# Kernel tuning notes

Measured on AMD Instinct MI355X. Metric: run time of the kernel, lower is better.

## Reference

```python
import jax, jax.numpy as jnp
import numpy as np

B, V, E, W = 1024, 50257, 128, 4  # batch, vocab, embed, CBOW window

def setup_inputs() -> dict:
    key = jax.random.key(0)
    k1, k2, k3, k4 = jax.random.split(key, 4)
    # near-one-hot averaged bag-of-words: 2*W context indices per row, each weighted 1/(2*W)
    ctx_idx = jax.random.randint(k1, (B, 2 * W), 0, V)
    xs = jnp.zeros((B, V), dtype=jnp.float32).at[jnp.arange(B)[:, None], ctx_idx].add(1.0 / (2 * W))
    metric = jax.random.normal(k2, (E, E), dtype=jnp.float32)  # unused by forward, kept for signature fidelity
    EMBEDM = jax.random.normal(k3, (V, E), dtype=jnp.float32)
    embed2vocab = jax.random.normal(k4, (E, V), dtype=jnp.float32)
    return {"xs": xs, "metric": metric, "EMBEDM": EMBEDM, "embed2vocab": embed2vocab}

def reference(xs, metric, EMBEDM, embed2vocab):
    # [B,V] @ [V,E] -> [B,E]  (gather+average in disguise: xs is sparse n-hot)
    xsembeds = xs @ EMBEDM
    # [B,E] @ [E,V] -> [B,V], then row-wise log_softmax
    xsouts = xsembeds @ embed2vocab
    return jax.nn.log_softmax(xsouts, axis=1)
```

## Files before the change

kernel.cpp:

```cpp
#include <hip/hip_runtime.h>
#include <hip/hip_bf16.h>

#define B_ROWS 1024
#define V_DIM 50257
#define E_DIM 128
#define V_PAD 50304
#define NCT 786

typedef __attribute__((ext_vector_type(8))) short short8;
typedef __attribute__((ext_vector_type(4))) float float4v;

__global__ void k0_transpose(const float* __restrict__ e2v,
                             __hip_bfloat16* __restrict__ e2vT) {
    __shared__ float t[32][33];
    const int v0 = blockIdx.x * 32;
    const int k0 = blockIdx.y * 32;
    const int c = threadIdx.x & 31;
    const int r = threadIdx.x >> 5;
#pragma unroll
    for (int i = 0; i < 4; ++i) {
        const int k = k0 + r + i * 8;
        const int v = v0 + c;
        t[r + i * 8][c] = (v < V_DIM) ? e2v[(size_t)k * V_DIM + v] : 0.0f;
    }
    __syncthreads();
#pragma unroll
    for (int i = 0; i < 4; ++i) {
        const int rv = r + i * 8;
        e2vT[(size_t)(v0 + rv) * E_DIM + k0 + c] = __float2bfloat16(t[c][rv]);
    }
}

__global__ void k1_embed(const float* __restrict__ xs,
                         const float* __restrict__ EM,
                         __hip_bfloat16* __restrict__ xse) {
    const int b = blockIdx.x;
    const int tid = threadIdx.x;
    __shared__ int nzv[64];
    __shared__ float nzval[64];
    __shared__ int nzcount;
    if (tid == 0) nzcount = 0;
    __syncthreads();

    const size_t base = (size_t)b * V_DIM;
    auto note = [&](int v, float val) {
        if (val != 0.0f) {
            int s = atomicAdd(&nzcount, 1);
            if (s < 64) { nzv[s] = v; nzval[s] = val; }
        }
    };

    const int h = (int)((4 - (base & 3)) & 3);
    if (tid < h) note(tid, xs[base + tid]);
    const int n4 = (V_DIM - h) >> 2;
    const float4* xv = reinterpret_cast<const float4*>(xs + base + h);
#pragma unroll 4
    for (int j = tid; j < n4; j += 256) {
        float4 x = xv[j];
        if (x.x != 0.0f || x.y != 0.0f || x.z != 0.0f || x.w != 0.0f) {
            const int v = h + 4 * j;
            note(v + 0, x.x);
            note(v + 1, x.y);
            note(v + 2, x.z);
            note(v + 3, x.w);
        }
    }
    for (int i = h + n4 * 4 + tid; i < V_DIM; i += 256) note(i, xs[base + i]);
    __syncthreads();

    int cnt = nzcount;
    if (cnt > 64) cnt = 64;
    if (tid < E_DIM) {
        float a = 0.0f;
        for (int s = 0; s < cnt; ++s)
            a += nzval[s] * EM[(size_t)nzv[s] * E_DIM + tid];
        xse[(size_t)b * E_DIM + tid] = __float2bfloat16(a);
    }
}

template <bool PASS2>
__global__ __launch_bounds__(256) void gemm_tile(
        const __hip_bfloat16* __restrict__ xse,
        const __hip_bfloat16* __restrict__ e2vT,
        float* __restrict__ psum,
        const float* __restrict__ stats,
        float* __restrict__ out) {
    __shared__ __align__(16) unsigned short Bs[64][136];
    const int tid = threadIdx.x;
    const int v0 = blockIdx.x * 64;
    const int m0 = blockIdx.y * 128;

    const unsigned short* gA = reinterpret_cast<const unsigned short*>(xse);
    const unsigned short* gB = reinterpret_cast<const unsigned short*>(e2vT);

    int4 g[4];
#pragma unroll
    for (int i = 0; i < 4; ++i) {
        const int p = tid + i * 256;
        const int row = p >> 4;
        const int kc = (p & 15) << 3;
        g[i] = *reinterpret_cast<const int4*>(gB + (size_t)(v0 + row) * E_DIM + kc);
    }

    const int w = tid >> 6;
    const int lane = tid & 63;
    const int q = lane >> 4;
    const int l16 = lane & 15;
    const int wm = w * 32;

    short8 af[2][4];
#pragma unroll
    for (int mi = 0; mi < 2; ++mi)
#pragma unroll
        for (int kt = 0; kt < 4; ++kt)
            af[mi][kt] = *reinterpret_cast<const short8*>(
                gA + (size_t)(m0 + wm + mi * 16 + l16) * E_DIM + kt * 32 + q * 8);

#pragma unroll
    for (int i = 0; i < 4; ++i) {
        const int p = tid + i * 256;
        const int row = p >> 4;
        const int kc = (p & 15) << 3;
        *reinterpret_cast<int4*>(&Bs[row][kc]) = g[i];
    }
    __syncthreads();

    float4v acc[2][4];
#pragma unroll
    for (int mi = 0; mi < 2; ++mi)
#pragma unroll
        for (int ni = 0; ni < 4; ++ni)
            acc[mi][ni] = (float4v){0.0f, 0.0f, 0.0f, 0.0f};

#pragma unroll
    for (int kt = 0; kt < 4; ++kt) {
        const int ko = kt * 32 + q * 8;
#pragma unroll
        for (int ni = 0; ni < 4; ++ni) {
            short8 bf = *reinterpret_cast<const short8*>(&Bs[ni * 16 + l16][ko]);
            acc[0][ni] = __builtin_amdgcn_mfma_f32_16x16x32_bf16(af[0][kt], bf, acc[0][ni], 0, 0, 0);
            acc[1][ni] = __builtin_amdgcn_mfma_f32_16x16x32_bf16(af[1][kt], bf, acc[1][ni], 0, 0, 0);
        }
    }

    if constexpr (!PASS2) {
        const bool full = (v0 + 64 <= V_DIM);
#pragma unroll
        for (int mi = 0; mi < 2; ++mi) {
#pragma unroll
            for (int r = 0; r < 4; ++r) {
                float s;
                if (full) {
                    s = __expf(acc[mi][0][r]) + __expf(acc[mi][1][r]) +
                        __expf(acc[mi][2][r]) + __expf(acc[mi][3][r]);
                } else {
                    s = 0.0f;
#pragma unroll
                    for (int ni = 0; ni < 4; ++ni)
                        if (v0 + ni * 16 + l16 < V_DIM) s += __expf(acc[mi][ni][r]);
                }
                s += __shfl_xor(s, 1);
                s += __shfl_xor(s, 2);
                s += __shfl_xor(s, 4);
                s += __shfl_xor(s, 8);
                if (l16 == 0) {
                    const int row = m0 + wm + mi * 16 + q * 4 + r;
                    psum[(size_t)row * NCT + blockIdx.x] = s;
                }
            }
        }
    } else {
#pragma unroll
        for (int mi = 0; mi < 2; ++mi) {
            const int rbase = m0 + wm + mi * 16 + q * 4;
            float l[4];
#pragma unroll
            for (int r = 0; r < 4; ++r) l[r] = stats[rbase + r];
#pragma unroll
            for (int ni = 0; ni < 4; ++ni) {
                const int col = v0 + ni * 16 + l16;
                if (col < V_DIM) {
#pragma unroll
                    for (int r = 0; r < 4; ++r)
                        out[(size_t)(rbase + r) * V_DIM + col] = acc[mi][ni][r] - l[r];
                }
            }
        }
    }
}

__global__ void kc_combine(const float* __restrict__ psum,
                           float* __restrict__ stats) {
    const int b = blockIdx.x;
    const int lane = threadIdx.x;
    float s = 0.0f;
    for (int j = lane; j < NCT; j += 64) s += psum[(size_t)b * NCT + j];
#pragma unroll
    for (int d = 1; d < 64; d <<= 1) s += __shfl_xor(s, d);
    if (lane == 0) stats[b] = __logf(s);
}

extern "C" void kernel_launch(void* const* d_in, const int* in_sizes, int n_in,
                              void* d_out, int out_size, void* d_ws, size_t ws_size,
                              hipStream_t stream) {
    const float* xs  = (const float*)d_in[0];
    const float* EM  = (const float*)d_in[2];
    const float* e2v = (const float*)d_in[3];
    float* out = (float*)d_out;

    char* ws = (char*)d_ws;
    __hip_bfloat16* e2vT = (__hip_bfloat16*)ws;
    size_t off = (size_t)V_PAD * E_DIM * 2;
    __hip_bfloat16* xse = (__hip_bfloat16*)(ws + off);
    off += (size_t)B_ROWS * E_DIM * 2;
    float* psum = (float*)(ws + off);
    off += (size_t)B_ROWS * NCT * 4;
    float* stats = (float*)(ws + off);

    k0_transpose<<<dim3(V_PAD / 32, E_DIM / 32), dim3(256), 0, stream>>>(e2v, e2vT);
    k1_embed<<<dim3(B_ROWS), dim3(256), 0, stream>>>(xs, EM, xse);
    gemm_tile<false><<<dim3(NCT, B_ROWS / 128), dim3(256), 0, stream>>>(
        xse, e2vT, psum, nullptr, nullptr);
    kc_combine<<<dim3(B_ROWS), dim3(64), 0, stream>>>(psum, stats);
    gemm_tile<true><<<dim3(NCT, B_ROWS / 128), dim3(256), 0, stream>>>(
        xse, e2vT, nullptr, stats, out);
}
```

Baseline: 472.3 us.

## Fuse all stages into one persistent cooperative kernel with grid syncs

Replaces the five separate launches (transpose, embed, sum pass, combine, output pass) with a single cooperative persistent kernel that steps through the stages with grid-wide syncs. Each block handles a contiguous range of jobs ordered so consecutive jobs reuse the same vocab tile already loaded in shared memory, which avoids reloading the B tile for all 8 row panels. The aim is to remove launch gaps and tail effects between kernels. The cost is grid-sync overhead, a grid capped at 1024 blocks, and higher shared-memory use per block. The old multi-kernel path remains as a fallback if the cooperative launch fails.

New measurement: 673.9 us. 42.7% more time.

```diff
diff --git a/kernel.cpp b/kernel.cpp
--- a/kernel.cpp
+++ b/kernel.cpp
@@ -1,14 +1,262 @@
 #include <hip/hip_runtime.h>
 #include <hip/hip_bf16.h>
+#include <hip/hip_cooperative_groups.h>
+
+namespace cg = cooperative_groups;
 
 #define B_ROWS 1024
 #define V_DIM 50257
 #define E_DIM 128
 #define V_PAD 50304
 #define NCT 786
+#define NPANEL 8
+#define NJOBS (NCT * NPANEL)
+#define NTX 1572
+#define NTJOBS (NTX * 4)
+#define MAXGRID 1024
 
 typedef __attribute__((ext_vector_type(8))) short short8;
 typedef __attribute__((ext_vector_type(4))) float float4v;
+
+__global__ __launch_bounds__(256, 4) void fused(
+        const float* __restrict__ xs,
+        const float* __restrict__ EM,
+        const float* __restrict__ e2v,
+        __hip_bfloat16* __restrict__ e2vT,
+        __hip_bfloat16* __restrict__ xse,
+        float* __restrict__ psum,
+        float* __restrict__ stats,
+        float* __restrict__ out) {
+    __shared__ __align__(16) unsigned short Bs[64][136];
+    __shared__ float t[32][33];
+    __shared__ int nzv[64];
+    __shared__ float nzval[64];
+    __shared__ int nzcount;
+
+    const int bid = blockIdx.x;
+    const int nblk = gridDim.x;
+    const int tid = threadIdx.x;
+    const int w = tid >> 6;
+    const int lane = tid & 63;
+    const int q = lane >> 4;
+    const int l16 = lane & 15;
+    const int wm = w * 32;
+    cg::grid_group gg = cg::this_grid();
+
+    for (int job = bid; job < NTJOBS; job += nblk) {
+        const int y = job / NTX;
+        const int x = job - y * NTX;
+        const int v0 = x * 32, k0 = y * 32;
+        const int c = tid & 31, r = tid >> 5;
+#pragma unroll
+        for (int i = 0; i < 4; ++i) {
+            const int k = k0 + r + i * 8;
+            const int v = v0 + c;
+            t[r + i * 8][c] = (v < V_DIM) ? e2v[(size_t)k * V_DIM + v] : 0.0f;
+        }
+        __syncthreads();
+#pragma unroll
+        for (int i = 0; i < 4; ++i) {
+            const int rv = r + i * 8;
+            e2vT[(size_t)(v0 + rv) * E_DIM + k0 + c] = __float2bfloat16(t[c][rv]);
+        }
+        __syncthreads();
+    }
+
+    for (int b = bid; b < B_ROWS; b += nblk) {
+        if (tid == 0) nzcount = 0;
+        __syncthreads();
+        const size_t base = (size_t)b * V_DIM;
+        auto note = [&](int v, float val) {
+            if (val != 0.0f) {
+                int s = atomicAdd(&nzcount, 1);
+                if (s < 64) { nzv[s] = v; nzval[s] = val; }
+            }
+        };
+        const int h = (int)((4 - (base & 3)) & 3);
+        if (tid < h) note(tid, xs[base + tid]);
+        const int n4 = (V_DIM - h) >> 2;
+        const float4* xv = reinterpret_cast<const float4*>(xs + base + h);
+#pragma unroll 4
+        for (int j = tid; j < n4; j += 256) {
+            float4 x = xv[j];
+            if (x.x != 0.0f || x.y != 0.0f || x.z != 0.0f || x.w != 0.0f) {
+                const int v = h + 4 * j;
+                note(v + 0, x.x);
+                note(v + 1, x.y);
+                note(v + 2, x.z);
+                note(v + 3, x.w);
+            }
+        }
+        for (int i = h + n4 * 4 + tid; i < V_DIM; i += 256) note(i, xs[base + i]);
+        __syncthreads();
+        int cnt = nzcount;
+        if (cnt > 64) cnt = 64;
+        if (tid < E_DIM) {
+            float a = 0.0f;
+            for (int s = 0; s < cnt; ++s)
+                a += nzval[s] * EM[(size_t)nzv[s] * E_DIM + tid];
+            xse[(size_t)b * E_DIM + tid] = __float2bfloat16(a);
+        }
+        __syncthreads();
+    }
+
+    gg.sync();
+
+    const unsigned short* gA = reinterpret_cast<const unsigned short*>(xse);
+    const unsigned short* gB = reinterpret_cast<const unsigned short*>(e2vT);
+    const int js = (int)(((long long)bid * NJOBS) / nblk);
+    const int je = (int)(((long long)(bid + 1) * NJOBS) / nblk);
+
+    {
+        int vcur = -1;
+        for (int job = js; job < je; ++job) {
+            const int v = job >> 3;
+            const int p = job & 7;
+            const int v0 = v * 64, m0 = p * 128;
+            if (v != vcur) {
+                __syncthreads();
+#pragma unroll
+                for (int i = 0; i < 4; ++i) {
+                    const int pp = tid + i * 256;
+                    const int row = pp >> 4;
+                    const int kc = (pp & 15) << 3;
+                    *reinterpret_cast<int4*>(&Bs[row][kc]) =
+                        *reinterpret_cast<const int4*>(gB + (size_t)(v0 + row) * E_DIM + kc);
+                }
+                __syncthreads();
+                vcur = v;
+            }
+            short8 af[2][4];
+#pragma unroll
+            for (int mi = 0; mi < 2; ++mi)
+#pragma unroll
+                for (int kt = 0; kt < 4; ++kt)
+                    af[mi][kt] = *reinterpret_cast<const short8*>(
+                        gA + (size_t)(m0 + wm + mi * 16 + l16) * E_DIM + kt * 32 + q * 8);
+
+            float4v acc[2][4];
+#pragma unroll
+            for (int mi = 0; mi < 2; ++mi)
+#pragma unroll
+                for (int ni = 0; ni < 4; ++ni)
+                    acc[mi][ni] = (float4v){0.0f, 0.0f, 0.0f, 0.0f};
+#pragma unroll
+            for (int kt = 0; kt < 4; ++kt) {
+                const int ko = kt * 32 + q * 8;
+#pragma unroll
+                for (int ni = 0; ni < 4; ++ni) {
+                    short8 bf = *reinterpret_cast<const short8*>(&Bs[ni * 16 + l16][ko]);
+                    acc[0][ni] = __builtin_amdgcn_mfma_f32_16x16x32_bf16(af[0][kt], bf, acc[0][ni], 0, 0, 0);
+                    acc[1][ni] = __builtin_amdgcn_mfma_f32_16x16x32_bf16(af[1][kt], bf, acc[1][ni], 0, 0, 0);
+                }
+            }
+            const bool full = (v0 + 64 <= V_DIM);
+#pragma unroll
+            for (int mi = 0; mi < 2; ++mi) {
+#pragma unroll
+                for (int r = 0; r < 4; ++r) {
+                    float s;
+                    if (full) {
+                        s = __expf(acc[mi][0][r]) + __expf(acc[mi][1][r]) +
+                            __expf(acc[mi][2][r]) + __expf(acc[mi][3][r]);
+                    } else {
+                        s = 0.0f;
+#pragma unroll
+                        for (int ni = 0; ni < 4; ++ni)
+                            if (v0 + ni * 16 + l16 < V_DIM) s += __expf(acc[mi][ni][r]);
+                    }
+                    s += __shfl_xor(s, 1);
+                    s += __shfl_xor(s, 2);
+                    s += __shfl_xor(s, 4);
+                    s += __shfl_xor(s, 8);
+                    if (l16 == 0) {
+                        const int row = m0 + wm + mi * 16 + q * 4 + r;
+                        psum[(size_t)row * NCT + v] = s;
+                    }
+                }
+            }
+        }
+    }
+
+    gg.sync();
+
+    for (int b = bid; b < B_ROWS; b += nblk) {
+        float s = 0.0f;
+        for (int j = tid; j < NCT; j += 256) s += psum[(size_t)b * NCT + j];
+#pragma unroll
+        for (int d = 1; d < 64; d <<= 1) s += __shfl_xor(s, d);
+        float* red = reinterpret_cast<float*>(t);
+        if (lane == 0) red[w] = s;
+        __syncthreads();
+        if (tid == 0) stats[b] = __logf(red[0] + red[1] + red[2] + red[3]);
+        __syncthreads();
+    }
+
+    gg.sync();
+
+    {
+        int vcur = -1;
+        for (int job = js; job < je; ++job) {
+            const int v = job >> 3;
+            const int p = job & 7;
+            const int v0 = v * 64, m0 = p * 128;
+            if (v != vcur) {
+                __syncthreads();
+#pragma unroll
+                for (int i = 0; i < 4; ++i) {
+                    const int pp = tid + i * 256;
+                    const int row = pp >> 4;
+                    const int kc = (pp & 15) << 3;
+                    *reinterpret_cast<int4*>(&Bs[row][kc]) =
+                        *reinterpret_cast<const int4*>(gB + (size_t)(v0 + row) * E_DIM + kc);
+                }
+                __syncthreads();
+                vcur = v;
+            }
+            short8 af[2][4];
+#pragma unroll
+            for (int mi = 0; mi < 2; ++mi)
+#pragma unroll
+                for (int kt = 0; kt < 4; ++kt)
+                    af[mi][kt] = *reinterpret_cast<const short8*>(
+                        gA + (size_t)(m0 + wm + mi * 16 + l16) * E_DIM + kt * 32 + q * 8);
+
+            float4v acc[2][4];
+#pragma unroll
+            for (int mi = 0; mi < 2; ++mi)
+#pragma unroll
+                for (int ni = 0; ni < 4; ++ni)
+                    acc[mi][ni] = (float4v){0.0f, 0.0f, 0.0f, 0.0f};
+#pragma unroll
+            for (int kt = 0; kt < 4; ++kt) {
+                const int ko = kt * 32 + q * 8;
+#pragma unroll
+                for (int ni = 0; ni < 4; ++ni) {
+                    short8 bf = *reinterpret_cast<const short8*>(&Bs[ni * 16 + l16][ko]);
+                    acc[0][ni] = __builtin_amdgcn_mfma_f32_16x16x32_bf16(af[0][kt], bf, acc[0][ni], 0, 0, 0);
+                    acc[1][ni] = __builtin_amdgcn_mfma_f32_16x16x32_bf16(af[1][kt], bf, acc[1][ni], 0, 0, 0);
+                }
+            }
+#pragma unroll
+            for (int mi = 0; mi < 2; ++mi) {
+                const int rbase = m0 + wm + mi * 16 + q * 4;
+                float l[4];
+#pragma unroll
+                for (int r = 0; r < 4; ++r) l[r] = stats[rbase + r];
+#pragma unroll
+                for (int ni = 0; ni < 4; ++ni) {
+                    const int col = v0 + ni * 16 + l16;
+                    if (col < V_DIM) {
+#pragma unroll
+                        for (int r = 0; r < 4; ++r)
+                            out[(size_t)(rbase + r) * V_DIM + col] = acc[mi][ni][r] - l[r];
+                    }
+                }
+            }
+        }
+    }
+}
 
 __global__ void k0_transpose(const float* __restrict__ e2v,
                              __hip_bfloat16* __restrict__ e2vT) {
@@ -41,7 +289,6 @@
     __shared__ int nzcount;
     if (tid == 0) nzcount = 0;
     __syncthreads();
-
     const size_t base = (size_t)b * V_DIM;
     auto note = [&](int v, float val) {
         if (val != 0.0f) {
@@ -49,7 +296,6 @@
             if (s < 64) { nzv[s] = v; nzval[s] = val; }
         }
     };
-
     const int h = (int)((4 - (base & 3)) & 3);
     if (tid < h) note(tid, xs[base + tid]);
     const int n4 = (V_DIM - h) >> 2;
@@ -67,7 +313,6 @@
     }
     for (int i = h + n4 * 4 + tid; i < V_DIM; i += 256) note(i, xs[base + i]);
     __syncthreads();
-
     int cnt = nzcount;
     if (cnt > 64) cnt = 64;
     if (tid < E_DIM) {
@@ -89,10 +334,8 @@
     const int tid = threadIdx.x;
     const int v0 = blockIdx.x * 64;
     const int m0 = blockIdx.y * 128;
-
     const unsigned short* gA = reinterpret_cast<const unsigned short*>(xse);
     const unsigned short* gB = reinterpret_cast<const unsigned short*>(e2vT);
-
     int4 g[4];
 #pragma unroll
     for (int i = 0; i < 4; ++i) {
@@ -101,13 +344,11 @@
         const int kc = (p & 15) << 3;
         g[i] = *reinterpret_cast<const int4*>(gB + (size_t)(v0 + row) * E_DIM + kc);
     }
-
     const int w = tid >> 6;
     const int lane = tid & 63;
     const int q = lane >> 4;
     const int l16 = lane & 15;
     const int wm = w * 32;
-
     short8 af[2][4];
 #pragma unroll
     for (int mi = 0; mi < 2; ++mi)
@@ -115,7 +356,6 @@
         for (int kt = 0; kt < 4; ++kt)
             af[mi][kt] = *reinterpret_cast<const short8*>(
                 gA + (size_t)(m0 + wm + mi * 16 + l16) * E_DIM + kt * 32 + q * 8);
-
 #pragma unroll
     for (int i = 0; i < 4; ++i) {
         const int p = tid + i * 256;
@@ -124,14 +364,12 @@
         *reinterpret_cast<int4*>(&Bs[row][kc]) = g[i];
     }
     __syncthreads();
-
     float4v acc[2][4];
 #pragma unroll
     for (int mi = 0; mi < 2; ++mi)
 #pragma unroll
         for (int ni = 0; ni < 4; ++ni)
             acc[mi][ni] = (float4v){0.0f, 0.0f, 0.0f, 0.0f};
-
 #pragma unroll
     for (int kt = 0; kt < 4; ++kt) {
         const int ko = kt * 32 + q * 8;
@@ -142,7 +380,6 @@
             acc[1][ni] = __builtin_amdgcn_mfma_f32_16x16x32_bf16(af[1][kt], bf, acc[1][ni], 0, 0, 0);
         }
     }
-
     if constexpr (!PASS2) {
         const bool full = (v0 + 64 <= V_DIM);
 #pragma unroll
@@ -217,11 +454,28 @@
     off += (size_t)B_ROWS * NCT * 4;
     float* stats = (float*)(ws + off);
 
-    k0_transpose<<<dim3(V_PAD / 32, E_DIM / 32), dim3(256), 0, stream>>>(e2v, e2vT);
-    k1_embed<<<dim3(B_ROWS), dim3(256), 0, stream>>>(xs, EM, xse);
-    gemm_tile<false><<<dim3(NCT, B_ROWS / 128), dim3(256), 0, stream>>>(
-        xse, e2vT, psum, nullptr, nullptr);
-    kc_combine<<<dim3(B_ROWS), dim3(64), 0, stream>>>(psum, stats);
-    gemm_tile<true><<<dim3(NCT, B_ROWS / 128), dim3(256), 0, stream>>>(
-        xse, e2vT, nullptr, stats, out);
-}
+    int nbPerCU = 0;
+    hipError_t oe = hipOccupancyMaxActiveBlocksPerMultiprocessor(
+        &nbPerCU, (const void*)fused, 256, 0);
+    int nCU = 256;
+    hipDeviceGetAttribute(&nCU, hipDeviceAttributeMultiprocessorCount, 0);
+    int grid = MAXGRID;
+    if (oe == hipSuccess && nbPerCU > 0) {
+        const int cap = nbPerCU * nCU;
+        if (grid > cap) grid = cap;
+    }
+
+    void* kargs[] = {(void*)&xs, (void*)&EM, (void*)&e2v, (void*)&e2vT,
+                     (void*)&xse, (void*)&psum, (void*)&stats, (void*)&out};
+    hipError_t le = hipLaunchCooperativeKernel((const void*)fused, dim3(grid),
+                                               dim3(256), kargs, 0, stream);
+    if (le != hipSuccess) {
+        k0_transpose<<<dim3(V_PAD / 32, E_DIM / 32), dim3(256), 0, stream>>>(e2v, e2vT);
+        k1_embed<<<dim3(B_ROWS), dim3(256), 0, stream>>>(xs, EM, xse);
+        gemm_tile<false><<<dim3(NCT, B_ROWS / 128), dim3(256), 0, stream>>>(
+            xse, e2vT, psum, nullptr, nullptr);
+        kc_combine<<<dim3(B_ROWS), dim3(64), 0, stream>>>(psum, stats);
+        gemm_tile<true><<<dim3(NCT, B_ROWS / 128), dim3(256), 0, stream>>>(
+            xse, e2vT, nullptr, stats, out);
+    }
+}
```

## Merge prep kernels and replace partial-sum combine with atomic row sums

Applied to the files above, without the earlier changes.

Fuses the transpose and embedding-gather kernels into one launch that splits work by block index, and zeroes a row-sum buffer in the same launch. The first GEMM pass now atomically accumulates exp sums per row instead of writing per-tile partials, so the separate combine kernel is removed and the second pass takes the log inline. This drops two kernel launches and the partial-sum buffer traffic, in exchange for global float atomics (786 per row) with nondeterministic summation order and a redundant log per tile.

Result: slower. 593.2 us (+25.6%).

```diff
diff --git a/kernel.cpp b/kernel.cpp
--- a/kernel.cpp
+++ b/kernel.cpp
@@ -6,75 +6,83 @@
 #define E_DIM 128
 #define V_PAD 50304
 #define NCT 786
+#define NTX 1572
+#define NTJOBS (NTX * 4)
 
 typedef __attribute__((ext_vector_type(8))) short short8;
 typedef __attribute__((ext_vector_type(4))) float float4v;
 
-__global__ void k0_transpose(const float* __restrict__ e2v,
-                             __hip_bfloat16* __restrict__ e2vT) {
-    __shared__ float t[32][33];
-    const int v0 = blockIdx.x * 32;
-    const int k0 = blockIdx.y * 32;
-    const int c = threadIdx.x & 31;
-    const int r = threadIdx.x >> 5;
-#pragma unroll
-    for (int i = 0; i < 4; ++i) {
-        const int k = k0 + r + i * 8;
-        const int v = v0 + c;
-        t[r + i * 8][c] = (v < V_DIM) ? e2v[(size_t)k * V_DIM + v] : 0.0f;
-    }
-    __syncthreads();
-#pragma unroll
-    for (int i = 0; i < 4; ++i) {
-        const int rv = r + i * 8;
-        e2vT[(size_t)(v0 + rv) * E_DIM + k0 + c] = __float2bfloat16(t[c][rv]);
-    }
-}
-
-__global__ void k1_embed(const float* __restrict__ xs,
-                         const float* __restrict__ EM,
-                         __hip_bfloat16* __restrict__ xse) {
-    const int b = blockIdx.x;
+
+__global__ void ka_prep(const float* __restrict__ e2v,
+                        const float* __restrict__ xs,
+                        const float* __restrict__ EM,
+                        __hip_bfloat16* __restrict__ e2vT,
+                        __hip_bfloat16* __restrict__ xse,
+                        float* __restrict__ rowsum) {
     const int tid = threadIdx.x;
-    __shared__ int nzv[64];
-    __shared__ float nzval[64];
-    __shared__ int nzcount;
-    if (tid == 0) nzcount = 0;
-    __syncthreads();
-
-    const size_t base = (size_t)b * V_DIM;
-    auto note = [&](int v, float val) {
-        if (val != 0.0f) {
-            int s = atomicAdd(&nzcount, 1);
-            if (s < 64) { nzv[s] = v; nzval[s] = val; }
-        }
-    };
-
-    const int h = (int)((4 - (base & 3)) & 3);
-    if (tid < h) note(tid, xs[base + tid]);
-    const int n4 = (V_DIM - h) >> 2;
-    const float4* xv = reinterpret_cast<const float4*>(xs + base + h);
+    if (blockIdx.x < NTJOBS) {
+        __shared__ float t[32][33];
+        if (blockIdx.x < 4 && tid < B_ROWS / 4)
+            rowsum[blockIdx.x * (B_ROWS / 4) + tid] = 0.0f;
+        const int job = blockIdx.x;
+        const int y = job >> 11;
+        const int yy = job / NTX;
+        const int xx = job - yy * NTX;
+        (void)y;
+        const int v0 = xx * 32, k0 = yy * 32;
+        const int c = tid & 31;
+        const int r = tid >> 5;
+#pragma unroll
+        for (int i = 0; i < 4; ++i) {
+            const int k = k0 + r + i * 8;
+            const int v = v0 + c;
+            t[r + i * 8][c] = (v < V_DIM) ? e2v[(size_t)k * V_DIM + v] : 0.0f;
+        }
+        __syncthreads();
+#pragma unroll
+        for (int i = 0; i < 4; ++i) {
+            const int rv = r + i * 8;
+            e2vT[(size_t)(v0 + rv) * E_DIM + k0 + c] = __float2bfloat16(t[c][rv]);
+        }
+    } else {
+        const int b = blockIdx.x - NTJOBS;
+        __shared__ int nzv[64];
+        __shared__ float nzval[64];
+        __shared__ int nzcount;
+        if (tid == 0) nzcount = 0;
+        __syncthreads();
+        const size_t base = (size_t)b * V_DIM;
+        auto note = [&](int v, float val) {
+            if (val != 0.0f) {
+                int s = atomicAdd(&nzcount, 1);
+                if (s < 64) { nzv[s] = v; nzval[s] = val; }
+            }
+        };
+        const int h = (int)((4 - (base & 3)) & 3);
+        if (tid < h) note(tid, xs[base + tid]);
+        const int n4 = (V_DIM - h) >> 2;
+        const float4* xv = reinterpret_cast<const float4*>(xs + base + h);
 #pragma unroll 4
-    for (int j = tid; j < n4; j += 256) {
-        float4 x = xv[j];
-        if (x.x != 0.0f || x.y != 0.0f || x.z != 0.0f || x.w != 0.0f) {
-            const int v = h + 4 * j;
-            note(v + 0, x.x);
-            note(v + 1, x.y);
-            note(v + 2, x.z);
-            note(v + 3, x.w);
-        }
-    }
-    for (int i = h + n4 * 4 + tid; i < V_DIM; i += 256) note(i, xs[base + i]);
-    __syncthreads();
-
-    int cnt = nzcount;
-    if (cnt > 64) cnt = 64;
-    if (tid < E_DIM) {
-        float a = 0.0f;
-        for (int s = 0; s < cnt; ++s)
-            a += nzval[s] * EM[(size_t)nzv[s] * E_DIM + tid];
-        xse[(size_t)b * E_DIM + tid] = __float2bfloat16(a);
+        for (int j = tid; j < n4; j += 256) {
+            float4 x = xv[j];
+            if (x.x != 0.0f || x.y != 0.0f || x.z != 0.0f || x.w != 0.0f) {
+                const int v = h + 4 * j;
+                note(v + 0, x.x);
+                note(v + 1, x.y);
+                note(v + 2, x.z);
+                note(v + 3, x.w);
+            }
+        }
+        for (int i = h + n4 * 4 + tid; i < V_DIM; i += 256) note(i, xs[base + i]);
+        __syncthreads();
+        int cnt = nzcount;
+        if (cnt > 64) cnt = 64;
+        if (tid < E_DIM) {
+            float a = 0.0f;
+            for (int s = 0; s < cnt; ++s)
+                a += nzval[s] * EM[(size_t)nzv[s] * E_DIM + tid];
+            xse[(size_t)b * E_DIM + tid] = __float2bfloat16(a);
+        }
     }
 }
 
@@ -82,14 +90,12 @@
 __global__ __launch_bounds__(256) void gemm_tile(
         const __hip_bfloat16* __restrict__ xse,
         const __hip_bfloat16* __restrict__ e2vT,
-        float* __restrict__ psum,
-        const float* __restrict__ stats,
+        float* __restrict__ rowsum,
         float* __restrict__ out) {
     __shared__ __align__(16) unsigned short Bs[64][136];
     const int tid = threadIdx.x;
     const int v0 = blockIdx.x * 64;
     const int m0 = blockIdx.y * 128;
-
     const unsigned short* gA = reinterpret_cast<const unsigned short*>(xse);
     const unsigned short* gB = reinterpret_cast<const unsigned short*>(e2vT);
 
@@ -101,13 +107,11 @@
         const int kc = (p & 15) << 3;
         g[i] = *reinterpret_cast<const int4*>(gB + (size_t)(v0 + row) * E_DIM + kc);
     }
-
     const int w = tid >> 6;
     const int lane = tid & 63;
     const int q = lane >> 4;
     const int l16 = lane & 15;
     const int wm = w * 32;
-
     short8 af[2][4];
 #pragma unroll
     for (int mi = 0; mi < 2; ++mi)
@@ -115,7 +119,6 @@
         for (int kt = 0; kt < 4; ++kt)
             af[mi][kt] = *reinterpret_cast<const short8*>(
                 gA + (size_t)(m0 + wm + mi * 16 + l16) * E_DIM + kt * 32 + q * 8);
-
 #pragma unroll
     for (int i = 0; i < 4; ++i) {
         const int p = tid + i * 256;
@@ -131,7 +134,6 @@
 #pragma unroll
         for (int ni = 0; ni < 4; ++ni)
             acc[mi][ni] = (float4v){0.0f, 0.0f, 0.0f, 0.0f};
-
 #pragma unroll
     for (int kt = 0; kt < 4; ++kt) {
         const int ko = kt * 32 + q * 8;
@@ -165,7 +167,7 @@
                 s += __shfl_xor(s, 8);
                 if (l16 == 0) {
                     const int row = m0 + wm + mi * 16 + q * 4 + r;
-                    psum[(size_t)row * NCT + blockIdx.x] = s;
+                    atomicAdd(&rowsum[row], s);
                 }
             }
         }
@@ -175,7 +177,7 @@
             const int rbase = m0 + wm + mi * 16 + q * 4;
             float l[4];
 #pragma unroll
-            for (int r = 0; r < 4; ++r) l[r] = stats[rbase + r];
+            for (int r = 0; r < 4; ++r) l[r] = __logf(rowsum[rbase + r]);
 #pragma unroll
             for (int ni = 0; ni < 4; ++ni) {
                 const int col = v0 + ni * 16 + l16;
@@ -187,17 +189,6 @@
             }
         }
     }
-}
-
-__global__ void kc_combine(const float* __restrict__ psum,
-                           float* __restrict__ stats) {
-    const int b = blockIdx.x;
-    const int lane = threadIdx.x;
-    float s = 0.0f;
-    for (int j = lane; j < NCT; j += 64) s += psum[(size_t)b * NCT + j];
-#pragma unroll
-    for (int d = 1; d < 64; d <<= 1) s += __shfl_xor(s, d);
-    if (lane == 0) stats[b] = __logf(s);
 }
 
 extern "C" void kernel_launch(void* const* d_in, const int* in_sizes, int n_in,
@@ -213,15 +204,12 @@
     size_t off = (size_t)V_PAD * E_DIM * 2;
     __hip_bfloat16* xse = (__hip_bfloat16*)(ws + off);
     off += (size_t)B_ROWS * E_DIM * 2;
-    float* psum = (float*)(ws + off);
-    off += (size_t)B_ROWS * NCT * 4;
-    float* stats = (float*)(ws + off);
-
-    k0_transpose<<<dim3(V_PAD / 32, E_DIM / 32), dim3(256), 0, stream>>>(e2v, e2vT);
-    k1_embed<<<dim3(B_ROWS), dim3(256), 0, stream>>>(xs, EM, xse);
+    float* rowsum = (float*)(ws + off);
+
+    ka_prep<<<dim3(NTJOBS + B_ROWS), dim3(256), 0, stream>>>(
+        e2v, xs, EM, e2vT, xse, rowsum);
     gemm_tile<false><<<dim3(NCT, B_ROWS / 128), dim3(256), 0, stream>>>(
-        xse, e2vT, psum, nullptr, nullptr);
-    kc_combine<<<dim3(B_ROWS), dim3(64), 0, stream>>>(psum, stats);
+        xse, e2vT, rowsum, nullptr);
     gemm_tile<true><<<dim3(NCT, B_ROWS / 128), dim3(256), 0, stream>>>(
-        xse, e2vT, nullptr, stats, out);
+        xse, e2vT, rowsum, out);
 }
```
